# Kernel optimization log

Measured on AMD Instinct MI355X. Metric: run time of the kernel, lower is better.

The kernel has to match this reference:

```python
import jax, jax.numpy as jnp
import numpy as np

N_NODES = 100000
N_EDGES = 1600000
F_IN = 64
N_HID = 64
N_CLS = 40
K = 2  # kernel_size, degree-1 open B-spline in 1-D pseudo-coordinate


def setup_inputs() -> dict:
    key = jax.random.key(0)
    ks = jax.random.split(key, 8)
    x = jax.random.normal(ks[0], (N_NODES, F_IN), dtype=jnp.float32)
    edge_index = jax.random.randint(ks[1], (2, N_EDGES), 0, N_NODES, dtype=jnp.int32)
    edge_attr = jax.random.uniform(ks[2], (N_EDGES, 1), dtype=jnp.float32)
    s1 = 1.0 / np.sqrt(F_IN)
    s2 = 1.0 / np.sqrt(N_HID)
    W1 = jax.random.normal(ks[3], (K, F_IN, N_HID), dtype=jnp.float32) * s1
    root1 = jax.random.normal(ks[4], (F_IN, N_HID), dtype=jnp.float32) * s1
    b1 = jnp.zeros((N_HID,), dtype=jnp.float32)
    W2 = jax.random.normal(ks[5], (K, N_HID, N_CLS), dtype=jnp.float32) * s2
    root2 = jax.random.normal(ks[6], (N_HID, N_CLS), dtype=jnp.float32) * s2
    b2 = jnp.zeros((N_CLS,), dtype=jnp.float32)
    return {"x": x, "edge_index": edge_index, "edge_attr": edge_attr,
            "W1": W1, "root1": root1, "b1": b1,
            "W2": W2, "root2": root2, "b2": b2}


def spline_conv(x, src, dst, u, W, root, b):
    """SplineConv, dim=1, kernel_size=2, degree=1, open spline, aggr='mean'.

    Degree-1 open spline with K=2: frac = u*(K-1) = u, basis weights are
    (1-u) at kernel index 0 and u at kernel index 1 for u in [0,1).
    Transform nodes once per kernel index, then gather+mix per edge (cheaper
    and mathematically identical to per-edge matmuls since basis scalars
    commute with the linear map).
    """
    h = jnp.einsum('nf,kfo->kno', x, W)  # [K, N, out]
    b1f = u[:, 0]                        # fractional basis weight, [E]
    msg = (1.0 - b1f)[:, None] * h[0][src] + b1f[:, None] * h[1][src]  # [E, out]
    agg = jax.ops.segment_sum(msg, dst, num_segments=x.shape[0])
    deg = jax.ops.segment_sum(jnp.ones_like(b1f), dst, num_segments=x.shape[0])
    agg = agg / jnp.maximum(deg, 1.0)[:, None]  # mean aggregation
    return agg + x @ root + b


def reference(x, edge_index, edge_attr, W1, root1, b1, W2, root2, b2):
    src, dst = edge_index[0], edge_index[1]
    # eval mode: F.dropout(training=False) is identity
    h = jax.nn.elu(spline_conv(x, src, dst, edge_attr, W1, root1, b1))
    out = spline_conv(h, src, dst, edge_attr, W2, root2, b2)
    return jax.nn.log_softmax(out, axis=1)
```

## Files before the change

kernel.cpp:

```cpp
#include <hip/hip_runtime.h>
#include <math.h>

#define N_NODES 100000
#define N_EDGES 1600000
#define NB_SCAN 391
#define CHUNK 4096
#define NCHA 391
#define NBUK 256
#define DPB 391
#define BSTRIDE 7168

typedef __attribute__((ext_vector_type(8))) short bf16x8;
typedef __attribute__((ext_vector_type(4))) float f32x4;

__device__ __forceinline__ unsigned short f2bf(float f) {
    union { float f; unsigned u; } v; v.f = f;
    unsigned r = v.u + 0x7FFF + ((v.u >> 16) & 1);
    return (unsigned short)(r >> 16);
}
__device__ __forceinline__ float bf2f(unsigned short b) {
    union { unsigned u; float f; } v; v.u = ((unsigned)b) << 16;
    return v.f;
}

__global__ void x2bf16_kernel(const float* __restrict__ x,
                              unsigned short* __restrict__ xb) {
    int i = blockIdx.x * 256 + threadIdx.x;
    if (i >= N_NODES * 16) return;
    float4 v = reinterpret_cast<const float4*>(x)[i];
    ushort4 o;
    o.x = f2bf(v.x); o.y = f2bf(v.y); o.z = f2bf(v.z); o.w = f2bf(v.w);
    reinterpret_cast<ushort4*>(xb)[i] = o;
}

__global__ void wt_kernel(const float* __restrict__ W, const float* __restrict__ root,
                          unsigned short* __restrict__ Wt, int COUT, int total) {
    int i = blockIdx.x * 256 + threadIdx.x;
    if (i >= total) return;
    int c = i / 192;
    int k = i - c * 192;
    float v = 0.0f;
    if (c < COUT)
        v = (k < 128) ? W[(k >> 6) * 64 * COUT + (k & 63) * COUT + c]
                      : root[(k - 128) * COUT + c];
    Wt[i] = f2bf(v);
}

__global__ __launch_bounds__(256) void bin_edges(const int* __restrict__ ei,
                                                 const float* __restrict__ ea,
                                                 int* __restrict__ bucket_cur,
                                                 int2* __restrict__ binned) {
    __shared__ int hist[NBUK];
    __shared__ int lbase[NBUK];
    __shared__ int lcur[NBUK];
    __shared__ int gbase[NBUK];
    __shared__ int2 stage[CHUNK];
    __shared__ unsigned char sbkt[CHUNK];
    int tid = threadIdx.x;
    int e0 = blockIdx.x * CHUNK;
    int nval = min(CHUNK, N_EDGES - e0);

    if (tid < NBUK) hist[tid] = 0;
    __syncthreads();
    for (int j = tid; j < nval; j += 256)
        atomicAdd(&hist[ei[N_EDGES + e0 + j] / DPB], 1);
    __syncthreads();
    if (tid < NBUK) lbase[tid] = hist[tid];
    __syncthreads();
    for (int off = 1; off < NBUK; off <<= 1) {
        int v = (tid < NBUK && tid >= off) ? lbase[tid - off] : 0;
        __syncthreads();
        if (tid < NBUK) lbase[tid] += v;
        __syncthreads();
    }
    if (tid < NBUK) {
        int ex = lbase[tid] - hist[tid];
        lbase[tid] = ex;
        lcur[tid]  = ex;
        gbase[tid] = atomicAdd(&bucket_cur[tid], hist[tid]);
    }
    __syncthreads();
    for (int j = tid; j < nval; j += 256) {
        int e = e0 + j;
        int d = ei[N_EDGES + e];
        int b = d / DPB;
        int dl = d - b * DPB;
        float u = ea[e];
        int uq = min((int)(u * 65536.0f + 0.5f), 65535);
        int pos = atomicAdd(&lcur[b], 1);
        stage[pos] = make_int2(ei[e], (uq << 16) | dl);
        sbkt[pos] = (unsigned char)b;
    }
    __syncthreads();
    for (int j = tid; j < nval; j += 256) {
        int b = sbkt[j];
        int gp = gbase[b] + (j - lbase[b]);
        if (gp < BSTRIDE)
            binned[(size_t)b * BSTRIDE + gp] = stage[j];
    }
}

__global__ __launch_bounds__(512) void bucket_sort(const int* __restrict__ bucket_cur,
                                                   const int2* __restrict__ binned,
                                                   int2* __restrict__ rec,
                                                   int* __restrict__ rowptr,
                                                   int* __restrict__ cnt_g) {
    __shared__ int cntA[512];
    __shared__ int cntB[512];
    __shared__ int2 stage[BSTRIDE];
    int tid = threadIdx.x;
    int b = blockIdx.x;

    cntA[tid] = (tid < NBUK) ? bucket_cur[tid] : 0;
    __syncthreads();
    cntB[tid] = cntA[tid];
    __syncthreads();
    for (int off = 1; off < 512; off <<= 1) {
        int v = (tid >= off) ? cntB[tid - off] : 0;
        __syncthreads();
        cntB[tid] += v;
        __syncthreads();
    }
    int base = (b == 0) ? 0 : cntB[b - 1];
    int m = min(cntA[b], BSTRIDE);
    __syncthreads();

    cntA[tid] = 0;
    __syncthreads();
    const int2* bin = binned + (size_t)b * BSTRIDE;
    for (int j = tid; j < m; j += 512)
        atomicAdd(&cntA[bin[j].y & 1023], 1);
    __syncthreads();
    cntB[tid] = cntA[tid];
    __syncthreads();
    for (int off = 1; off < 512; off <<= 1) {
        int v = (tid >= off) ? cntB[tid - off] : 0;
        __syncthreads();
        cntB[tid] += v;
        __syncthreads();
    }
    {
        int ex = cntB[tid] - cntA[tid];
        int d = b * DPB + tid;
        if (tid < DPB && d < N_NODES) {
            rowptr[d] = base + ex;
            cnt_g[d]  = cntA[tid];
        }
        __syncthreads();
        cntB[tid] = ex;
    }
    __syncthreads();
    for (int j = tid; j < m; j += 512) {
        int2 r = bin[j];
        int dl = r.y & 1023;
        float u = ((unsigned)r.y >> 16) * (1.0f / 65536.0f);
        int pos = atomicAdd(&cntB[dl], 1);
        if (pos < BSTRIDE) stage[pos] = make_int2(r.x, __float_as_int(u));
    }
    __syncthreads();
    for (int j = tid; j < m; j += 512)
        rec[base + j] = stage[j];
}

__global__ __launch_bounds__(256) void pull_agg(
        const int* __restrict__ rowptr, const int* __restrict__ cnt,
        const int2* __restrict__ rec, const unsigned short* __restrict__ featb,
        unsigned short* __restrict__ s01b) {
    int wave_id = (blockIdx.x * 256 + threadIdx.x) >> 6;
    int lane = threadIdx.x & 63;
    int fg = lane & 7;
    int eg = lane >> 3;
    int n = wave_id * 8 + eg;
    bool valid = n < N_NODES;
    int start = 0, deg = 0;
    if (valid) { start = rowptr[n]; deg = cnt[n]; }
    int end = start + deg;
    const bf16x8* f8 = reinterpret_cast<const bf16x8*>(featb);
    float s[8], a1[8];
#pragma unroll
    for (int k = 0; k < 8; ++k) { s[k] = 0.0f; a1[k] = 0.0f; }

    int i = start;
    if (i < end) {
        int2   r0 = rec[i];
        bf16x8 v0 = f8[((size_t)(unsigned)r0.x << 3) + fg];
        while (true) {
            int inext = i + 1;
            bool more = inext < end;
            int2   r1;
            bf16x8 v1;
            if (more) {
                r1 = rec[inext];
                v1 = f8[((size_t)(unsigned)r1.x << 3) + fg];
            }
            float u = __int_as_float(r0.y);
#pragma unroll
            for (int k = 0; k < 8; ++k) {
                float v = bf2f((unsigned short)v0[k]);
                s[k] += v;
                a1[k] = fmaf(u, v, a1[k]);
            }
            if (!more) break;
            r0 = r1; v0 = v1; i = inext;
        }
    }
    if (valid) {
        float dinv = 1.0f / fmaxf((float)deg, 1.0f);
        bf16x8 o0, o1;
#pragma unroll
        for (int k = 0; k < 8; ++k) {
            o0[k] = (short)f2bf((s[k] - a1[k]) * dinv);
            o1[k] = (short)f2bf(a1[k] * dinv);
        }
        *reinterpret_cast<bf16x8*>(s01b + (size_t)n * 128 + fg * 8) = o0;
        *reinterpret_cast<bf16x8*>(s01b + (size_t)n * 128 + 64 + fg * 8) = o1;
    }
}

template<int COUT, int CT, int ACT>
__global__ __launch_bounds__(256) void gemm_mfma(
        const unsigned short* __restrict__ s01b,
        const unsigned short* __restrict__ featb,
        const unsigned short* __restrict__ Wt,
        const float* __restrict__ bias, void* __restrict__ outv) {
    int lane = threadIdx.x & 63;
    int wave = threadIdx.x >> 6;
    int l15  = lane & 15;
    int g    = lane >> 4;
    int nodebase = blockIdx.x * 256 + wave * 64;

    f32x4 acc[4][CT];
#pragma unroll
    for (int rt = 0; rt < 4; ++rt)
#pragma unroll
        for (int ct = 0; ct < CT; ++ct) acc[rt][ct] = (f32x4){0.f, 0.f, 0.f, 0.f};

#pragma unroll
    for (int ks = 0; ks < 6; ++ks) {
        int kk = ks * 32 + g * 8;
        bf16x8 zfrag[4];
#pragma unroll
        for (int rt = 0; rt < 4; ++rt) {
            int n = nodebase + rt * 16 + l15;
            if (n >= N_NODES) n = N_NODES - 1;
            const unsigned short* p = (kk < 128)
                ? (s01b + (size_t)n * 128 + kk)
                : (featb + (size_t)n * 64 + (kk - 128));
            zfrag[rt] = *reinterpret_cast<const bf16x8*>(p);
        }
        bf16x8 wfrag[CT];
#pragma unroll
        for (int ct = 0; ct < CT; ++ct)
            wfrag[ct] = *reinterpret_cast<const bf16x8*>(Wt + (size_t)(ct * 16 + l15) * 192 + kk);
#pragma unroll
        for (int rt = 0; rt < 4; ++rt)
#pragma unroll
            for (int ct = 0; ct < CT; ++ct)
                acc[rt][ct] = __builtin_amdgcn_mfma_f32_16x16x32_bf16(
                    wfrag[ct], zfrag[rt], acc[rt][ct], 0, 0, 0);
    }

    f32x4 bv[CT];
#pragma unroll
    for (int ct = 0; ct < CT; ++ct) {
        int base = ct * 16 + g * 4;
        if (base + 4 <= COUT) {
            float4 b = *reinterpret_cast<const float4*>(bias + base);
            bv[ct] = (f32x4){b.x, b.y, b.z, b.w};
        } else {
            bv[ct] = (f32x4){0.f, 0.f, 0.f, 0.f};
        }
    }

    if (ACT == 1) {
        unsigned short* out = (unsigned short*)outv;
#pragma unroll
        for (int rt = 0; rt < 4; ++rt) {
            int n = nodebase + rt * 16 + l15;
            if (n >= N_NODES) continue;
#pragma unroll
            for (int ct = 0; ct < CT; ++ct) {
                f32x4 v = acc[rt][ct] + bv[ct];
                ushort4 o;
                float e;
                e = v[0]; o.x = f2bf(e > 0.f ? e : expm1f(e));
                e = v[1]; o.y = f2bf(e > 0.f ? e : expm1f(e));
                e = v[2]; o.z = f2bf(e > 0.f ? e : expm1f(e));
                e = v[3]; o.w = f2bf(e > 0.f ? e : expm1f(e));
                *reinterpret_cast<ushort4*>(out + (size_t)n * 64 + ct * 16 + g * 4) = o;
            }
        }
    } else {
        float* out = (float*)outv;
#pragma unroll
        for (int rt = 0; rt < 4; ++rt) {
            int n = nodebase + rt * 16 + l15;
            float v[CT * 4];
            float m = -3.4e38f;
#pragma unroll
            for (int ct = 0; ct < CT; ++ct)
#pragma unroll
                for (int r = 0; r < 4; ++r) {
                    int ch = ct * 16 + g * 4 + r;
                    float t = acc[rt][ct][r] + bv[ct][r];
                    v[ct * 4 + r] = t;
                    if (ch < COUT) m = fmaxf(m, t);
                }
            m = fmaxf(m, __shfl_xor(m, 16));
            m = fmaxf(m, __shfl_xor(m, 32));
            float s = 0.0f;
#pragma unroll
            for (int ct = 0; ct < CT; ++ct)
#pragma unroll
                for (int r = 0; r < 4; ++r) {
                    int ch = ct * 16 + g * 4 + r;
                    if (ch < COUT) s += expf(v[ct * 4 + r] - m);
                }
            s += __shfl_xor(s, 16);
            s += __shfl_xor(s, 32);
            float lse = m + logf(s);
            if (n >= N_NODES) continue;
#pragma unroll
            for (int ct = 0; ct < CT; ++ct) {
                int base = ct * 16 + g * 4;
                if (base + 4 <= COUT) {
                    float4 o;
                    o.x = v[ct * 4 + 0] - lse;
                    o.y = v[ct * 4 + 1] - lse;
                    o.z = v[ct * 4 + 2] - lse;
                    o.w = v[ct * 4 + 3] - lse;
                    *reinterpret_cast<float4*>(out + (size_t)n * COUT + base) = o;
                }
            }
        }
    }
}

extern "C" void kernel_launch(void* const* d_in, const int* in_sizes, int n_in,
                              void* d_out, int out_size, void* d_ws, size_t ws_size,
                              hipStream_t stream) {
    const float* x     = (const float*)d_in[0];
    const int*   ei    = (const int*)d_in[1];
    const float* ea    = (const float*)d_in[2];
    const float* W1    = (const float*)d_in[3];
    const float* root1 = (const float*)d_in[4];
    const float* b1    = (const float*)d_in[5];
    const float* W2    = (const float*)d_in[6];
    const float* root2 = (const float*)d_in[7];
    const float* b2    = (const float*)d_in[8];
    float* out = (float*)d_out;

    char* p = (char*)d_ws;
    int*   bucket_cur = (int*)p;            p += 512 * 4;
    int2*  binned  = (int2*)p;              p += (size_t)NBUK * BSTRIDE * 8;
    int2*  rec     = (int2*)p;              p += (size_t)N_EDGES * 8;
    int*   rowptr  = (int*)p;               p += (size_t)N_NODES * 4;
    int*   cnt     = (int*)p;               p += (size_t)N_NODES * 4;
    unsigned short* s01b = (unsigned short*)p;  p += (size_t)N_NODES * 128 * 2;
    unsigned short* xb   = (unsigned short*)p;  p += (size_t)N_NODES * 64 * 2;
    unsigned short* hprb = (unsigned short*)p;  p += (size_t)N_NODES * 64 * 2;
    unsigned short* Wt1  = (unsigned short*)p;  p += (size_t)64 * 192 * 2;
    unsigned short* Wt2  = (unsigned short*)p;  p += (size_t)48 * 192 * 2;

    x2bf16_kernel<<<(N_NODES * 16) / 256, 256, 0, stream>>>(x, xb);
    wt_kernel<<<48, 256, 0, stream>>>(W1, root1, Wt1, 64, 64 * 192);
    wt_kernel<<<36, 256, 0, stream>>>(W2, root2, Wt2, 40, 48 * 192);
    hipMemsetAsync(bucket_cur, 0, 512 * 4, stream);

    bin_edges<<<NCHA, 256, 0, stream>>>(ei, ea, bucket_cur, binned);
    bucket_sort<<<NBUK, 512, 0, stream>>>(bucket_cur, binned, rec, rowptr, cnt);

    pull_agg<<<(N_NODES + 31) / 32, 256, 0, stream>>>(rowptr, cnt, rec, xb, s01b);
    gemm_mfma<64, 4, 1><<<NB_SCAN, 256, 0, stream>>>(s01b, xb, Wt1, b1, hprb);

    pull_agg<<<(N_NODES + 31) / 32, 256, 0, stream>>>(rowptr, cnt, rec, hprb, s01b);
    gemm_mfma<40, 3, 2><<<NB_SCAN, 256, 0, stream>>>(s01b, hprb, Wt2, b2, out);
}
```

Baseline: 181.7 us.

## Sort in-edges by source tile and unroll pull-aggregation gathers by four

The bucket sort now keys each record on destination plus a coarse source-range tile (four tiles of 25000 nodes), so a node's incoming edges are grouped by source region. The intent is more cache locality when feature rows are gathered. The pull aggregation loop is also unrolled to keep four gathers in flight per iteration, with clamped indices and masked math for the tail. This costs more shared memory for the larger key histogram and some redundant loads and FMAs on low-degree nodes.

```diff
diff --git a/kernel.cpp b/kernel.cpp
--- a/kernel.cpp
+++ b/kernel.cpp
@@ -9,6 +9,7 @@
 #define NBUK 256
 #define DPB 391
 #define BSTRIDE 7168
+#define TILE_N 25000
 
 typedef __attribute__((ext_vector_type(8))) short bf16x8;
 typedef __attribute__((ext_vector_type(4))) float f32x4;
@@ -105,56 +106,66 @@
                                                    int2* __restrict__ rec,
                                                    int* __restrict__ rowptr,
                                                    int* __restrict__ cnt_g) {
-    __shared__ int cntA[512];
-    __shared__ int cntB[512];
+    __shared__ int keycnt[1600];
+    __shared__ int tsum[512];
     __shared__ int2 stage[BSTRIDE];
     int tid = threadIdx.x;
     int b = blockIdx.x;
 
-    cntA[tid] = (tid < NBUK) ? bucket_cur[tid] : 0;
-    __syncthreads();
-    cntB[tid] = cntA[tid];
+    tsum[tid] = (tid < NBUK) ? bucket_cur[tid] : 0;
     __syncthreads();
     for (int off = 1; off < 512; off <<= 1) {
-        int v = (tid >= off) ? cntB[tid - off] : 0;
-        __syncthreads();
-        cntB[tid] += v;
-        __syncthreads();
-    }
-    int base = (b == 0) ? 0 : cntB[b - 1];
-    int m = min(cntA[b], BSTRIDE);
-    __syncthreads();
-
-    cntA[tid] = 0;
+        int v = (tid >= off) ? tsum[tid - off] : 0;
+        __syncthreads();
+        tsum[tid] += v;
+        __syncthreads();
+    }
+    int base = (b == 0) ? 0 : tsum[b - 1];
+    int m = min(bucket_cur[b], BSTRIDE);
+    __syncthreads();
+
+    for (int k = tid; k < 1600; k += 512) keycnt[k] = 0;
     __syncthreads();
     const int2* bin = binned + (size_t)b * BSTRIDE;
-    for (int j = tid; j < m; j += 512)
-        atomicAdd(&cntA[bin[j].y & 1023], 1);
-    __syncthreads();
-    cntB[tid] = cntA[tid];
-    __syncthreads();
-    for (int off = 1; off < 512; off <<= 1) {
-        int v = (tid >= off) ? cntB[tid - off] : 0;
-        __syncthreads();
-        cntB[tid] += v;
-        __syncthreads();
-    }
-    {
-        int ex = cntB[tid] - cntA[tid];
-        int d = b * DPB + tid;
-        if (tid < DPB && d < N_NODES) {
-            rowptr[d] = base + ex;
-            cnt_g[d]  = cntA[tid];
-        }
-        __syncthreads();
-        cntB[tid] = ex;
-    }
-    __syncthreads();
     for (int j = tid; j < m; j += 512) {
         int2 r = bin[j];
-        int dl = r.y & 1023;
+        int key = ((r.y & 1023) << 2) | ((unsigned)r.x / TILE_N);
+        atomicAdd(&keycnt[key], 1);
+    }
+    __syncthreads();
+    int k0 = tid << 2;
+    int c0 = 0, c1 = 0, c2 = 0, c3 = 0;
+    if (tid < DPB) {
+        c0 = keycnt[k0]; c1 = keycnt[k0 + 1];
+        c2 = keycnt[k0 + 2]; c3 = keycnt[k0 + 3];
+    }
+    int s4 = c0 + c1 + c2 + c3;
+    tsum[tid] = s4;
+    __syncthreads();
+    for (int off = 1; off < 512; off <<= 1) {
+        int v = (tid >= off) ? tsum[tid - off] : 0;
+        __syncthreads();
+        tsum[tid] += v;
+        __syncthreads();
+    }
+    if (tid < DPB) {
+        int p = tsum[tid] - s4;
+        int d = b * DPB + tid;
+        if (d < N_NODES) {
+            rowptr[d] = base + p;
+            cnt_g[d]  = s4;
+        }
+        keycnt[k0] = p;     p += c0;
+        keycnt[k0 + 1] = p; p += c1;
+        keycnt[k0 + 2] = p; p += c2;
+        keycnt[k0 + 3] = p;
+    }
+    __syncthreads();
+    for (int j = tid; j < m; j += 512) {
+        int2 r = bin[j];
+        int key = ((r.y & 1023) << 2) | ((unsigned)r.x / TILE_N);
         float u = ((unsigned)r.y >> 16) * (1.0f / 65536.0f);
-        int pos = atomicAdd(&cntB[dl], 1);
+        int pos = atomicAdd(&keycnt[key], 1);
         if (pos < BSTRIDE) stage[pos] = make_int2(r.x, __float_as_int(u));
     }
     __syncthreads();
@@ -175,35 +186,55 @@
     int start = 0, deg = 0;
     if (valid) { start = rowptr[n]; deg = cnt[n]; }
     int end = start + deg;
+    int il  = end - 1;
     const bf16x8* f8 = reinterpret_cast<const bf16x8*>(featb);
     float s[8], a1[8];
 #pragma unroll
     for (int k = 0; k < 8; ++k) { s[k] = 0.0f; a1[k] = 0.0f; }
 
-    int i = start;
-    if (i < end) {
-        int2   r0 = rec[i];
-        bf16x8 v0 = f8[((size_t)(unsigned)r0.x << 3) + fg];
+#define LD(IDX, R, V)                                              \
+    { int ic = min(IDX, il); R = rec[ic];                          \
+      V = f8[((size_t)(unsigned)R.x << 3) + fg]; }
+#define MATH(IDX, R, V)                                            \
+    { float mk = (IDX < end) ? 1.0f : 0.0f;                        \
+      float um = mk * __int_as_float(R.y);                         \
+      _Pragma("unroll")                                            \
+      for (int t = 0; t < 8; ++t) {                                \
+          float vv = bf2f((unsigned short)V[t]);                   \
+          s[t]  = fmaf(mk, vv, s[t]);                              \
+          a1[t] = fmaf(um, vv, a1[t]);                             \
+      } }
+
+    if (deg > 0) {
+        int i = start;
+        int2 r0, r1, r2, r3; bf16x8 v0, v1, v2, v3;
+        LD(i,     r0, v0)
+        LD(i + 1, r1, v1)
+        LD(i + 2, r2, v2)
+        LD(i + 3, r3, v3)
         while (true) {
-            int inext = i + 1;
-            bool more = inext < end;
-            int2   r1;
-            bf16x8 v1;
+            int j = i + 4;
+            bool more = j < end;
+            int2 q0, q1, q2, q3; bf16x8 w0, w1, w2, w3;
             if (more) {
-                r1 = rec[inext];
-                v1 = f8[((size_t)(unsigned)r1.x << 3) + fg];
+                LD(j,     q0, w0)
+                LD(j + 1, q1, w1)
+                LD(j + 2, q2, w2)
+                LD(j + 3, q3, w3)
             }
-            float u = __int_as_float(r0.y);
-#pragma unroll
-            for (int k = 0; k < 8; ++k) {
-                float v = bf2f((unsigned short)v0[k]);
-                s[k] += v;
-                a1[k] = fmaf(u, v, a1[k]);
-            }
+            MATH(i,     r0, v0)
+            MATH(i + 1, r1, v1)
+            MATH(i + 2, r2, v2)
+            MATH(i + 3, r3, v3)
             if (!more) break;
-            r0 = r1; v0 = v1; i = inext;
-        }
-    }
+            i = j;
+            r0 = q0; v0 = w0; r1 = q1; v1 = w1;
+            r2 = q2; v2 = w2; r3 = q3; v3 = w3;
+        }
+    }
+#undef LD
+#undef MATH
+
     if (valid) {
         float dinv = 1.0f / fmaxf((float)deg, 1.0f);
         bf16x8 o0, o1;
```

New measurement: 163.4 us. 10.1% less time.
